# Performance work log

Measured on AMD Instinct MI355X. Metric: run time of the kernel, lower is better.

The kernel has to match this reference:

```python
import jax, jax.numpy as jnp
import numpy as np

B, T, D, A = 64, 1024, 768, 128

def setup_inputs() -> dict:
    key = jax.random.key(0)
    k1, k2, k3 = jax.random.split(key, 3)
    x = jax.random.normal(k1, (B, T, D), dtype=jnp.float32)
    # glorot_normal-style scaling for the learned projections
    W1 = jax.random.normal(k2, (D, A), dtype=jnp.float32) * np.sqrt(2.0 / (D + A))
    W2 = jax.random.normal(k3, (A, T), dtype=jnp.float32) * np.sqrt(2.0 / (A + T))
    return {"x": x, "W1": W1, "W2": W2}

def reference(x, W1, W2):
    # x: [B, T, D], W1: [D, A], W2: [A, T]
    OA = jnp.tanh(jnp.einsum('btd,da->bta', x, W1))      # [B, T, A]
    OA = jnp.einsum('bta,as->bts', OA, W2)               # [B, T, T]
    OA = jax.nn.softmax(OA, axis=-2)                     # softmax over source-time axis
    # ot[b,s,d] = sum_t x[b,t,d] * OA[b,t,s]  (x^T @ OA, then transpose back)
    ot = jnp.einsum('btd,bts->bsd', x, OA)               # [B, T, D]
    return ot
```

## Files before the change

kernel.cpp:

```cpp
#include <hip/hip_runtime.h>
#include <math.h>

#define B_ 64
#define T_ 1024
#define D_ 768
#define A_ 128

typedef __attribute__((ext_vector_type(4))) float f32x4;
typedef __attribute__((ext_vector_type(8))) short s16x8;
typedef __attribute__((ext_vector_type(4))) short s16x4;

__device__ inline short f2b(float f) {
  union { float f; unsigned u; } v; v.f = f;
  unsigned r = (v.u + 0x7FFFu + ((v.u >> 16) & 1u)) >> 16;
  return (short)r;
}
__device__ inline float b2f(short s) {
  union { unsigned u; float f; } v; v.u = ((unsigned)(unsigned short)s) << 16;
  return v.f;
}

__device__ inline void gll16(const void* g, const void* lds) {
  __builtin_amdgcn_global_load_lds(
      (const __attribute__((address_space(1))) unsigned*)g,
      (__attribute__((address_space(3))) unsigned*)lds, 16, 0, 0);
}

__global__ __launch_bounds__(512, 2)
void g4_div(const short* __restrict__ Ag, const short* __restrict__ Bg,
            const float* __restrict__ Rs, float* __restrict__ Cg) {
  __shared__ __align__(16) short AS[2][16384];
  __shared__ __align__(16) short BS[2][16384];
  unsigned nwg = gridDim.x;
  unsigned L = blockIdx.x;
  unsigned xcd = L & 7u, base = L >> 3;
  unsigned q = nwg >> 3, r = nwg & 7u;
  unsigned id = (xcd < r ? xcd * (q + 1) : r * (q + 1) + (xcd - r) * q) + base;
  const int bz = id / 12;
  const int rem = id - bz * 12;
  const int by = rem / 3, bx = rem - (rem / 3) * 3;
  const int m0 = by * 256, n0 = bx * 256;

  const short* Ab = Ag + (size_t)bz * (T_ * T_);
  const short* Bb = Bg + (size_t)bz * (D_ * T_);
  const float* rsb = Rs + (size_t)bz * T_;
  float* Cb = Cg + (size_t)bz * (T_ * D_);

  const int tid = threadIdx.x;
  const int w = tid >> 6, lane = tid & 63;
  const int wr = w >> 2, wc = w & 3;
  const int lr = lane & 15, lq = lane >> 4;
  const int swzk = (lane & 7) ^ ((lane >> 3) & 7);
  const int abase = (wr * 128 + lr) * 64;
  const int bbase = (wc * 64 + lr) * 64;
  const int sx = lr & 7;
  const int sl0 = (lq ^ sx) * 8;
  const int sl1 = ((4 + lq) ^ sx) * 8;

  f32x4 acc[8][4] = {};
  s16x8 bq[4][2];

#define STG(dst, src, r0, kt)                                                  \
  { _Pragma("unroll")                                                          \
    for (int jj = 0; jj < 2; ++jj) {                                           \
      int rr = jj * 64 + w * 8 + (lane >> 3);                                  \
      gll16((src) + (size_t)((r0) + rr) * 1024 + (kt) + swzk * 8,              \
            (dst) + jj * 4096 + w * 512);                                      \
    } }

#define PHASE(P, Q, VM, STAGE)                                                 \
  {                                                                            \
    s16x8 a0_ = *(const s16x8*)&AS[P][abase + (2 * (Q)) * 1024 + sl0];         \
    s16x8 a1_ = *(const s16x8*)&AS[P][abase + (2 * (Q)) * 1024 + sl1];         \
    s16x8 a2_ = *(const s16x8*)&AS[P][abase + (2 * (Q) + 1) * 1024 + sl0];     \
    s16x8 a3_ = *(const s16x8*)&AS[P][abase + (2 * (Q) + 1) * 1024 + sl1];     \
    if ((Q) == 0) {                                                            \
      _Pragma("unroll")                                                        \
      for (int nf = 0; nf < 4; ++nf) {                                         \
        bq[nf][0] = *(const s16x8*)&BS[P][bbase + nf * 1024 + sl0];            \
        bq[nf][1] = *(const s16x8*)&BS[P][bbase + nf * 1024 + sl1];            \
      }                                                                        \
    }                                                                          \
    STAGE;                                                                     \
    VM;                                                                        \
    __builtin_amdgcn_s_barrier();                                              \
    asm volatile("s_waitcnt lgkmcnt(0)" ::: "memory");                         \
    __builtin_amdgcn_s_setprio(1);                                             \
    _Pragma("unroll")                                                          \
    for (int nf = 0; nf < 4; ++nf) {                                           \
      acc[2*(Q)][nf]   = __builtin_amdgcn_mfma_f32_16x16x32_bf16(a0_, bq[nf][0], acc[2*(Q)][nf], 0, 0, 0);   \
      acc[2*(Q)+1][nf] = __builtin_amdgcn_mfma_f32_16x16x32_bf16(a2_, bq[nf][0], acc[2*(Q)+1][nf], 0, 0, 0); \
    }                                                                          \
    _Pragma("unroll")                                                          \
    for (int nf = 0; nf < 4; ++nf) {                                           \
      acc[2*(Q)][nf]   = __builtin_amdgcn_mfma_f32_16x16x32_bf16(a1_, bq[nf][1], acc[2*(Q)][nf], 0, 0, 0);   \
      acc[2*(Q)+1][nf] = __builtin_amdgcn_mfma_f32_16x16x32_bf16(a3_, bq[nf][1], acc[2*(Q)+1][nf], 0, 0, 0); \
    }                                                                          \
    __builtin_amdgcn_s_setprio(0);                                             \
    __builtin_amdgcn_s_barrier();                                              \
  }

#define VM6 asm volatile("s_waitcnt vmcnt(6)" ::: "memory")
#define VM0 asm volatile("s_waitcnt vmcnt(0)" ::: "memory")
#define NOP (void)0

  STG(&BS[0][0],    Bb, n0,       0);
  STG(&BS[0][8192], Bb, n0 + 128, 0);
  STG(&AS[0][0],    Ab, m0,       0);
  STG(&AS[0][8192], Ab, m0 + 128, 0);
  STG(&BS[1][0],    Bb, n0,       64);
  STG(&BS[1][8192], Bb, n0 + 128, 64);
  STG(&AS[1][0],    Ab, m0,       64);
  VM6;
  __builtin_amdgcn_s_barrier();

  for (int j = 0; j < 7; ++j) {
    const int kb = j * 128;
    PHASE(0, 0, NOP, STG(&AS[1][8192], Ab, m0 + 128, kb + 64));
    PHASE(0, 1, NOP, STG(&BS[0][0],    Bb, n0,       kb + 128));
    PHASE(0, 2, NOP, STG(&BS[0][8192], Bb, n0 + 128, kb + 128));
    PHASE(0, 3, VM6, STG(&AS[0][0],    Ab, m0,       kb + 128));
    PHASE(1, 0, NOP, STG(&AS[0][8192], Ab, m0 + 128, kb + 128));
    PHASE(1, 1, NOP, STG(&BS[1][0],    Bb, n0,       kb + 192));
    PHASE(1, 2, NOP, STG(&BS[1][8192], Bb, n0 + 128, kb + 192));
    PHASE(1, 3, VM6, STG(&AS[1][0],    Ab, m0,       kb + 192));
  }
  PHASE(0, 0, NOP, STG(&AS[1][8192], Ab, m0 + 128, 960));
  PHASE(0, 1, NOP, NOP);
  PHASE(0, 2, NOP, NOP);
  PHASE(0, 3, VM0, NOP);
  PHASE(1, 0, NOP, NOP);
  PHASE(1, 1, NOP, NOP);
  PHASE(1, 2, NOP, NOP);
  PHASE(1, 3, NOP, NOP);

#undef STG
#undef PHASE
#undef VM6
#undef VM0
#undef NOP

#pragma unroll
  for (int mf = 0; mf < 8; ++mf) {
    f32x4 rsv = *(const f32x4*)&rsb[m0 + wr * 128 + mf * 16 + lq * 4];
    f32x4 inv;
#pragma unroll
    for (int qq = 0; qq < 4; ++qq) {
      float iv;
      asm("v_rcp_f32 %0, %1" : "=v"(iv) : "v"(rsv[qq]));
      inv[qq] = iv;
    }
#pragma unroll
    for (int nf = 0; nf < 4; ++nf) {
      int m = m0 + wr * 128 + mf * 16 + lq * 4;
      int n = n0 + wc * 64 + nf * 16 + lr;
#pragma unroll
      for (int qq = 0; qq < 4; ++qq)
        Cb[(size_t)(m + qq) * D_ + n] = acc[mf][nf][qq] * inv[qq];
    }
  }
}

template<int BK, bool BF32, bool TANH_, bool WT, bool OB16, bool EXPSUM, bool XT>
__global__ __launch_bounds__(256, 2)
void gemm_bt(const short* __restrict__ Ab, const void* __restrict__ Bv,
             void* __restrict__ Cv, float* __restrict__ Rs,
             short* __restrict__ Xt,
             int M, int N, int K,
             long sA, long sB, long sC, int gx, int gy) {
  constexpr int OPS = 128 * BK;
  constexpr int BOUNCE = 128 * 136;
  constexpr int BASE = (2 * OPS > BOUNCE ? 2 * OPS : BOUNCE);
  __shared__ __align__(16) short SMEM[BASE + (XT ? 64 * 136 : 0)];
  short* As = SMEM;
  short* Bs = SMEM + OPS;
  short* Ts = SMEM + 2 * OPS;

  unsigned nwg = gridDim.x;
  unsigned L = blockIdx.x;
  unsigned xcd = L & 7u, base = L >> 3;
  unsigned q = nwg >> 3, r = nwg & 7u;
  unsigned id = (xcd < r ? xcd * (q + 1) : r * (q + 1) + (xcd - r) * q) + base;
  const int gxy = gx * gy;
  const int bz = id / gxy;
  const int rem = id - bz * gxy;
  const int by = rem / gx;
  const int bx = rem - by * gx;

  const int tid = threadIdx.x;
  const int w = tid >> 6, lane = tid & 63;
  const int n0 = bx * 128, m0 = by * 128;
  const int wr = w >> 1, wc = w & 1;
  const int lr = lane & 15, lq = lane >> 4;
  const short* A = Ab + (size_t)sA * bz;
  const short* Bb16 = nullptr; const float* Bf32 = nullptr;
  if (BF32) Bf32 = (const float*)Bv + (size_t)sB * bz;
  else      Bb16 = (const short*)Bv + (size_t)sB * bz;
  short* Xtb = XT ? Xt + (size_t)bz * ((size_t)D_ * T_) : nullptr;

  f32x4 acc[4][4] = {};

  constexpr int LPR = BK / 8;
  constexpr int RPC = 64 / LPR;
  constexpr int CPT = BK / 16;
  const int rl = lane / LPR;
  const int cl = (lane % LPR) * 8;

  for (int k0 = 0; k0 < K; k0 += BK) {
    __syncthreads();
#pragma unroll
    for (int i = 0; i < CPT; ++i) {
      int chunk = w * CPT + i;
      int row = chunk * RPC + rl;
      gll16(A + (size_t)(m0 + row) * K + k0 + cl, As + chunk * 512);
    }
    s16x8 parr[4];
    if (!BF32) {
#pragma unroll
      for (int i = 0; i < CPT; ++i) {
        int chunk = w * CPT + i;
        int row = chunk * RPC + rl;
        gll16(Bb16 + (size_t)(n0 + row) * K + k0 + cl, Bs + chunk * 512);
      }
    } else {
#pragma unroll
      for (int u = 0; u < 4; ++u) {
        int c = tid * 4 + u;
        int row = c >> 3, k8 = c & 7;
        const float* gp = Bf32 + (size_t)(n0 + row) * K + k0 + k8 * 8;
        float4 f0 = *(const float4*)gp;
        float4 f1 = *(const float4*)(gp + 4);
        s16x8 p;
        p[0] = f2b(f0.x); p[1] = f2b(f0.y); p[2] = f2b(f0.z); p[3] = f2b(f0.w);
        p[4] = f2b(f1.x); p[5] = f2b(f1.y); p[6] = f2b(f1.z); p[7] = f2b(f1.w);
        parr[u] = p;
        *(s16x8*)&Bs[row * 64 + k8 * 8] = p;
      }
    }
    __syncthreads();
#pragma unroll
    for (int kk = 0; kk < BK / 32; ++kk) {
      s16x8 a[4], b[4];
#pragma unroll
      for (int mf = 0; mf < 4; ++mf)
        a[mf] = *(const s16x8*)&As[(wr * 64 + mf * 16 + lr) * BK + kk * 32 + lq * 8];
#pragma unroll
      for (int nf = 0; nf < 4; ++nf)
        b[nf] = *(const s16x8*)&Bs[(wc * 64 + nf * 16 + lr) * BK + kk * 32 + lq * 8];
#pragma unroll
      for (int mf = 0; mf < 4; ++mf)
#pragma unroll
        for (int nf = 0; nf < 4; ++nf)
          acc[mf][nf] = __builtin_amdgcn_mfma_f32_16x16x32_bf16(
              a[mf], b[nf], acc[mf][nf], 0, 0, 0);
    }
    if constexpr (XT) {
#pragma unroll
      for (int u = 0; u < 4; ++u) {
        int c = tid * 4 + u;
        int row = c >> 3, k8 = c & 7;
#pragma unroll
        for (int j = 0; j < 8; ++j) Ts[(k8 * 8 + j) * 136 + row] = parr[u][j];
      }
      __syncthreads();
#pragma unroll
      for (int u = 0; u < 4; ++u) {
        int task = tid + u * 256;
        int dd = task >> 4, t8 = task & 15;
        *(s16x8*)&Xtb[(size_t)(k0 + dd) * T_ + n0 + t8 * 8] =
            *(const s16x8*)&Ts[dd * 136 + t8 * 8];
      }
    }
  }

  if (WT && OB16) {
    __syncthreads();
    float psum[4] = {0.f, 0.f, 0.f, 0.f};
#pragma unroll
    for (int mf = 0; mf < 4; ++mf)
#pragma unroll
      for (int nf = 0; nf < 4; ++nf) {
        int ml = wr * 64 + mf * 16 + lq * 4;
        int nl = wc * 64 + nf * 16 + lr;
        s16x4 pk;
#pragma unroll
        for (int qq = 0; qq < 4; ++qq) {
          float v = acc[mf][nf][qq];
          if (TANH_) v = tanhf(v);
          if (EXPSUM) v = __expf(v);
          pk[qq] = f2b(v);
          if (EXPSUM) psum[nf] += b2f(pk[qq]);
        }
        *(s16x4*)&SMEM[nl * 136 + ml] = pk;
      }
    if (EXPSUM) {
      float* rs = Rs + (size_t)T_ * bz;
#pragma unroll
      for (int nf = 0; nf < 4; ++nf) {
        psum[nf] += __shfl_xor(psum[nf], 16);
        psum[nf] += __shfl_xor(psum[nf], 32);
      }
      if (lq == 0) {
#pragma unroll
        for (int nf = 0; nf < 4; ++nf)
          atomicAdd(&rs[n0 + wc * 64 + nf * 16 + lr], psum[nf]);
      }
    }
    __syncthreads();
    short* C = (short*)Cv + (size_t)sC * bz;
#pragma unroll
    for (int it = 0; it < 8; ++it) {
      int row = it * 16 + (tid >> 4);
      int col = (tid & 15) * 8;
      *(s16x8*)(C + (size_t)(n0 + row) * M + m0 + col) =
          *(const s16x8*)&SMEM[row * 136 + col];
    }
  } else if (WT) {
    float* C = (float*)Cv + (size_t)sC * bz;
#pragma unroll
    for (int mf = 0; mf < 4; ++mf)
#pragma unroll
      for (int nf = 0; nf < 4; ++nf) {
        int mbase = m0 + wr * 64 + mf * 16 + lq * 4;
        int n = n0 + wc * 64 + nf * 16 + lr;
#pragma unroll
        for (int qq = 0; qq < 4; ++qq) {
          float v = acc[mf][nf][qq];
          if (TANH_) v = tanhf(v);
          C[(size_t)n * M + mbase + qq] = v;
        }
      }
  } else {
    float* C = (float*)Cv + (size_t)sC * bz;
#pragma unroll
    for (int mf = 0; mf < 4; ++mf)
#pragma unroll
      for (int nf = 0; nf < 4; ++nf) {
        int m = m0 + wr * 64 + mf * 16 + lq * 4;
        int n = n0 + wc * 64 + nf * 16 + lr;
#pragma unroll
        for (int qq = 0; qq < 4; ++qq) {
          float v = acc[mf][nf][qq];
          if (TANH_) v = tanhf(v);
          C[(size_t)(m + qq) * N + n] = v;
        }
      }
  }
}

__global__ __launch_bounds__(256)
void transpose_cvt(const float* __restrict__ src, short* __restrict__ dst,
                   int R, int C) {
  __shared__ float sh[64][65];
  const int tid = threadIdx.x;
  const float* s = src + (size_t)blockIdx.z * R * C;
  short* d = dst + (size_t)blockIdx.z * R * C;
  const int r0 = blockIdx.y * 64, c0 = blockIdx.x * 64;
#pragma unroll
  for (int u = 0; u < 4; ++u) {
    int e = tid + u * 256;
    int rr = e >> 4, cc4 = (e & 15) * 4;
    float4 v = *(const float4*)&s[(size_t)(r0 + rr) * C + c0 + cc4];
    sh[rr][cc4 + 0] = v.x;
    sh[rr][cc4 + 1] = v.y;
    sh[rr][cc4 + 2] = v.z;
    sh[rr][cc4 + 3] = v.w;
  }
  __syncthreads();
#pragma unroll
  for (int u = 0; u < 4; ++u) {
    int e = tid + u * 256;
    int dr = e >> 4, tc4 = (e & 15) * 4;
    s16x4 pk;
#pragma unroll
    for (int j = 0; j < 4; ++j) pk[j] = f2b(sh[tc4 + j][dr]);
    *(s16x4*)&d[(size_t)(c0 + dr) * R + r0 + tc4] = pk;
  }
}

extern "C" void kernel_launch(void* const* d_in, const int* in_sizes, int n_in,
                              void* d_out, int out_size, void* d_ws, size_t ws_size,
                              hipStream_t stream) {
  const float* x  = (const float*)d_in[0];
  const float* W1 = (const float*)d_in[1];
  const float* W2 = (const float*)d_in[2];
  float* out = (float*)d_out;

  short* xt  = (short*)d_ws;
  short* W1t = xt + (size_t)B_ * D_ * T_;
  short* W2t = W1t + (size_t)A_ * D_;
  short* H   = W2t + (size_t)T_ * A_;
  float* rs  = (float*)(H + (size_t)B_ * T_ * A_);
  short* St  = (short*)(rs + (size_t)B_ * T_);
  size_t fixed_bytes = (size_t)((char*)St - (char*)xt);
  long avail = (long)ws_size - (long)fixed_bytes;
  long per_b = (long)T_ * T_ * sizeof(short);
  int chunk = (int)(avail > 0 ? avail / per_b : 0);
  if (chunk > B_) chunk = B_;
  if (chunk < 1) chunk = 1;

  hipMemsetAsync(rs, 0, (size_t)B_ * T_ * sizeof(float), stream);

  transpose_cvt<<<dim3(A_ / 64, D_ / 64, 1), 256, 0, stream>>>(W1, W1t, D_, A_);
  transpose_cvt<<<dim3(T_ / 64, A_ / 64, 1), 256, 0, stream>>>(W2, W2t, A_, T_);

  gemm_bt<64, true, true, true, true, false, true>
      <<<(T_ / 128) * (A_ / 128) * B_, 256, 0, stream>>>(
      W1t, x, H, nullptr, xt, A_, T_, D_, 0, (long)T_ * D_, (long)T_ * A_,
      T_ / 128, A_ / 128);

  for (int b0 = 0; b0 < B_; b0 += chunk) {
    int nb = B_ - b0; if (nb > chunk) nb = chunk;
    gemm_bt<128, false, false, true, true, true, false>
        <<<(T_ / 128) * (T_ / 128) * nb, 256, 0, stream>>>(
        H + (size_t)b0 * T_ * A_, W2t, St, rs + (size_t)b0 * T_, nullptr,
        T_, T_, A_, (long)T_ * A_, 0, (long)T_ * T_,
        T_ / 128, T_ / 128);
    g4_div<<<12 * nb, 512, 0, stream>>>(
        St, xt + (size_t)b0 * (size_t)D_ * T_, rs + (size_t)b0 * T_,
        out + (size_t)b0 * (size_t)T_ * D_);
  }
}
```

Baseline: 293.1 us.

## Merge GEMM main-loop phases into double phases with fewer barriers

```diff
diff --git a/kernel.cpp b/kernel.cpp
--- a/kernel.cpp
+++ b/kernel.cpp
@@ -68,39 +68,53 @@
             (dst) + jj * 4096 + w * 512);                                      \
     } }
 
-#define PHASE(P, Q, VM, STAGE)                                                 \
+#define PH2(P, Q0, VM, ...)                                                    \
   {                                                                            \
-    s16x8 a0_ = *(const s16x8*)&AS[P][abase + (2 * (Q)) * 1024 + sl0];         \
-    s16x8 a1_ = *(const s16x8*)&AS[P][abase + (2 * (Q)) * 1024 + sl1];         \
-    s16x8 a2_ = *(const s16x8*)&AS[P][abase + (2 * (Q) + 1) * 1024 + sl0];     \
-    s16x8 a3_ = *(const s16x8*)&AS[P][abase + (2 * (Q) + 1) * 1024 + sl1];     \
-    if ((Q) == 0) {                                                            \
+    s16x8 a0_ = *(const s16x8*)&AS[P][abase + (2 * (Q0)) * 1024 + sl0];        \
+    s16x8 a1_ = *(const s16x8*)&AS[P][abase + (2 * (Q0)) * 1024 + sl1];        \
+    s16x8 a2_ = *(const s16x8*)&AS[P][abase + (2 * (Q0) + 1) * 1024 + sl0];    \
+    s16x8 a3_ = *(const s16x8*)&AS[P][abase + (2 * (Q0) + 1) * 1024 + sl1];    \
+    if ((Q0) == 0) {                                                           \
       _Pragma("unroll")                                                        \
       for (int nf = 0; nf < 4; ++nf) {                                         \
         bq[nf][0] = *(const s16x8*)&BS[P][bbase + nf * 1024 + sl0];            \
         bq[nf][1] = *(const s16x8*)&BS[P][bbase + nf * 1024 + sl1];            \
       }                                                                        \
     }                                                                          \
-    STAGE;                                                                     \
+    __VA_ARGS__;                                                               \
     VM;                                                                        \
     __builtin_amdgcn_s_barrier();                                              \
     asm volatile("s_waitcnt lgkmcnt(0)" ::: "memory");                         \
     __builtin_amdgcn_s_setprio(1);                                             \
     _Pragma("unroll")                                                          \
     for (int nf = 0; nf < 4; ++nf) {                                           \
-      acc[2*(Q)][nf]   = __builtin_amdgcn_mfma_f32_16x16x32_bf16(a0_, bq[nf][0], acc[2*(Q)][nf], 0, 0, 0);   \
-      acc[2*(Q)+1][nf] = __builtin_amdgcn_mfma_f32_16x16x32_bf16(a2_, bq[nf][0], acc[2*(Q)+1][nf], 0, 0, 0); \
+      acc[2*(Q0)][nf]   = __builtin_amdgcn_mfma_f32_16x16x32_bf16(a0_, bq[nf][0], acc[2*(Q0)][nf], 0, 0, 0);   \
+      acc[2*(Q0)+1][nf] = __builtin_amdgcn_mfma_f32_16x16x32_bf16(a2_, bq[nf][0], acc[2*(Q0)+1][nf], 0, 0, 0); \
+    }                                                                          \
+    s16x8 a4_ = *(const s16x8*)&AS[P][abase + (2 * (Q0) + 2) * 1024 + sl0];    \
+    s16x8 a5_ = *(const s16x8*)&AS[P][abase + (2 * (Q0) + 2) * 1024 + sl1];    \
+    s16x8 a6_ = *(const s16x8*)&AS[P][abase + (2 * (Q0) + 3) * 1024 + sl0];    \
+    s16x8 a7_ = *(const s16x8*)&AS[P][abase + (2 * (Q0) + 3) * 1024 + sl1];    \
+    _Pragma("unroll")                                                          \
+    for (int nf = 0; nf < 4; ++nf) {                                           \
+      acc[2*(Q0)][nf]   = __builtin_amdgcn_mfma_f32_16x16x32_bf16(a1_, bq[nf][1], acc[2*(Q0)][nf], 0, 0, 0);   \
+      acc[2*(Q0)+1][nf] = __builtin_amdgcn_mfma_f32_16x16x32_bf16(a3_, bq[nf][1], acc[2*(Q0)+1][nf], 0, 0, 0); \
     }                                                                          \
     _Pragma("unroll")                                                          \
     for (int nf = 0; nf < 4; ++nf) {                                           \
-      acc[2*(Q)][nf]   = __builtin_amdgcn_mfma_f32_16x16x32_bf16(a1_, bq[nf][1], acc[2*(Q)][nf], 0, 0, 0);   \
-      acc[2*(Q)+1][nf] = __builtin_amdgcn_mfma_f32_16x16x32_bf16(a3_, bq[nf][1], acc[2*(Q)+1][nf], 0, 0, 0); \
+      acc[2*(Q0)+2][nf] = __builtin_amdgcn_mfma_f32_16x16x32_bf16(a4_, bq[nf][0], acc[2*(Q0)+2][nf], 0, 0, 0); \
+      acc[2*(Q0)+3][nf] = __builtin_amdgcn_mfma_f32_16x16x32_bf16(a6_, bq[nf][0], acc[2*(Q0)+3][nf], 0, 0, 0); \
+    }                                                                          \
+    _Pragma("unroll")                                                          \
+    for (int nf = 0; nf < 4; ++nf) {                                           \
+      acc[2*(Q0)+2][nf] = __builtin_amdgcn_mfma_f32_16x16x32_bf16(a5_, bq[nf][1], acc[2*(Q0)+2][nf], 0, 0, 0); \
+      acc[2*(Q0)+3][nf] = __builtin_amdgcn_mfma_f32_16x16x32_bf16(a7_, bq[nf][1], acc[2*(Q0)+3][nf], 0, 0, 0); \
     }                                                                          \
     __builtin_amdgcn_s_setprio(0);                                             \
     __builtin_amdgcn_s_barrier();                                              \
   }
 
-#define VM6 asm volatile("s_waitcnt vmcnt(6)" ::: "memory")
+#define VM4 asm volatile("s_waitcnt vmcnt(4)" ::: "memory")
 #define VM0 asm volatile("s_waitcnt vmcnt(0)" ::: "memory")
 #define NOP (void)0
 
@@ -110,33 +124,34 @@
   STG(&AS[0][8192], Ab, m0 + 128, 0);
   STG(&BS[1][0],    Bb, n0,       64);
   STG(&BS[1][8192], Bb, n0 + 128, 64);
-  STG(&AS[1][0],    Ab, m0,       64);
-  VM6;
+  VM4;
   __builtin_amdgcn_s_barrier();
 
   for (int j = 0; j < 7; ++j) {
     const int kb = j * 128;
-    PHASE(0, 0, NOP, STG(&AS[1][8192], Ab, m0 + 128, kb + 64));
-    PHASE(0, 1, NOP, STG(&BS[0][0],    Bb, n0,       kb + 128));
-    PHASE(0, 2, NOP, STG(&BS[0][8192], Bb, n0 + 128, kb + 128));
-    PHASE(0, 3, VM6, STG(&AS[0][0],    Ab, m0,       kb + 128));
-    PHASE(1, 0, NOP, STG(&AS[0][8192], Ab, m0 + 128, kb + 128));
-    PHASE(1, 1, NOP, STG(&BS[1][0],    Bb, n0,       kb + 192));
-    PHASE(1, 2, NOP, STG(&BS[1][8192], Bb, n0 + 128, kb + 192));
-    PHASE(1, 3, VM6, STG(&AS[1][0],    Ab, m0,       kb + 192));
-  }
-  PHASE(0, 0, NOP, STG(&AS[1][8192], Ab, m0 + 128, 960));
-  PHASE(0, 1, NOP, NOP);
-  PHASE(0, 2, NOP, NOP);
-  PHASE(0, 3, VM0, NOP);
-  PHASE(1, 0, NOP, NOP);
-  PHASE(1, 1, NOP, NOP);
-  PHASE(1, 2, NOP, NOP);
-  PHASE(1, 3, NOP, NOP);
+    PH2(0, 0, NOP,
+        STG(&AS[1][0],    Ab, m0,       kb + 64);
+        STG(&AS[1][8192], Ab, m0 + 128, kb + 64));
+    PH2(0, 2, VM4,
+        STG(&BS[0][0],    Bb, n0,       kb + 128);
+        STG(&BS[0][8192], Bb, n0 + 128, kb + 128));
+    PH2(1, 0, NOP,
+        STG(&AS[0][0],    Ab, m0,       kb + 128);
+        STG(&AS[0][8192], Ab, m0 + 128, kb + 128));
+    PH2(1, 2, VM4,
+        STG(&BS[1][0],    Bb, n0,       kb + 192);
+        STG(&BS[1][8192], Bb, n0 + 128, kb + 192));
+  }
+  PH2(0, 0, NOP,
+      STG(&AS[1][0],    Ab, m0,       960);
+      STG(&AS[1][8192], Ab, m0 + 128, 960));
+  PH2(0, 2, VM0, NOP);
+  PH2(1, 0, NOP, NOP);
+  PH2(1, 2, NOP, NOP);
 
 #undef STG
-#undef PHASE
-#undef VM6
+#undef PH2
+#undef VM4
 #undef VM0
 #undef NOP
 
```

Result: faster. 285.3 us (-2.7%).
